# Performance work log

Measured on AMD Instinct MI355X. Metric: run time of the kernel, lower is better.

The kernel has to match this reference:

```python
import jax, jax.numpy as jnp
import numpy as np
import math

B, D_MODEL, EMB, ORDER, SEQ = 4, 64, 33, 64, 256
TARGET, FAST_PCT, SLOW_PCT = 0.01, 0.3, 1.5


def _pos_emb(L, emb_dim):
    # PositionalEmbedding: t in [0,1], complex exponential bands
    t = jnp.linspace(0.0, 1.0, L)[None, :, None]                     # [1,L,1]
    bands = (emb_dim - 1) // 2
    t_r = jnp.linspace(0.0, L - 1.0, L)[None, :, None]
    w = 2.0 * math.pi * t_r / L
    f = jnp.linspace(1e-4, bands - 1.0, bands)[None, None]
    zc = jnp.exp(-1j * f * w)
    z = jnp.concatenate([t, zc.real, zc.imag], axis=-1)              # [1,L,emb_dim]
    return z.astype(jnp.float32), t.astype(jnp.float32)


def setup_inputs() -> dict:
    key = jax.random.key(0)
    ks = jax.random.split(key, 24)
    z, _ = _pos_emb(SEQ, EMB)

    def lin(k, fan_in, fan_out):
        return jax.random.normal(k, (fan_in, fan_out), jnp.float32) / np.sqrt(fan_in)

    inp = {
        'x': jax.random.normal(ks[0], (B, D_MODEL, SEQ, SEQ), jnp.float32),
        'z': z,
        'Xw1': lin(ks[1], EMB, ORDER), 'Xb1': jax.random.normal(ks[2], (ORDER,), jnp.float32) * 0.02,
        'Xw2': lin(ks[3], ORDER, ORDER), 'Xb2': jax.random.normal(ks[4], (ORDER,), jnp.float32) * 0.02,
        'Xw3': lin(ks[5], ORDER, ORDER), 'Xb3': jax.random.normal(ks[6], (ORDER,), jnp.float32) * 0.02,
        'Xwo': lin(ks[7], ORDER, D_MODEL),
        'Xfreq': jnp.ones((1, ORDER), jnp.float32),  # Sin freq, w=1, shared across layers
        'Yw1': lin(ks[8], EMB, ORDER), 'Yb1': jax.random.normal(ks[9], (ORDER,), jnp.float32) * 0.02,
        'Yw2': lin(ks[10], ORDER, ORDER), 'Yb2': jax.random.normal(ks[11], (ORDER,), jnp.float32) * 0.02,
        'Yw3': lin(ks[12], ORDER, ORDER), 'Yb3': jax.random.normal(ks[13], (ORDER,), jnp.float32) * 0.02,
        'Ywo': lin(ks[14], ORDER, D_MODEL),
        'Yfreq': jnp.ones((1, ORDER), jnp.float32),
        'bias': jax.random.normal(ks[15], (D_MODEL,), jnp.float32),
        'L': SEQ,
    }
    return inp


def _implicit_filter(z, w1, b1, w2, b2, w3, b3, wo, freq, t, deltas):
    # MLP with shared Sin activation, then exponential modulation (shift=0)
    h = jnp.sin(freq * (z @ w1 + b1))
    h = jnp.sin(freq * (h @ w2 + b2))
    h = jnp.sin(freq * (h @ w3 + b3))
    h = h @ wo                                   # [1,L,d_model]
    decay = jnp.exp(-t * jnp.abs(deltas))        # [1,L,d_model]
    return h * decay


def reference(x, z, Xw1, Xb1, Xw2, Xb2, Xw3, Xb3, Xwo, Xfreq,
              Yw1, Yb1, Yw2, Yb2, Yw3, Yb3, Ywo, Yfreq, bias, L):
    d_model = x.shape[1]
    t = jnp.linspace(0.0, 1.0, L)[None, :, None].astype(jnp.float32)
    max_dec = math.log(TARGET) / FAST_PCT
    min_dec = math.log(TARGET) / SLOW_PCT
    deltas = jnp.linspace(min_dec, max_dec, d_model)[None, None].astype(jnp.float32)

    hx = _implicit_filter(z, Xw1, Xb1, Xw2, Xb2, Xw3, Xb3, Xwo, Xfreq, t, deltas)
    hy = _implicit_filter(z, Yw1, Yb1, Yw2, Yb2, Yw3, Yb3, Ywo, Yfreq, t, deltas)
    # separable outer-product 2D kernel: [1,L,L,d_model] -> [d_model,L,L]
    k = jnp.einsum('ijk,imk->ijmk', hx, hy)[0]
    k = jnp.transpose(k, (2, 0, 1))

    fft_size = 2 * L
    k_f = jnp.fft.rfft2(k, s=(fft_size, fft_size)) / fft_size       # [D, 2L, L+1]
    u_f = jnp.fft.rfft2(x.astype(jnp.float32), s=(fft_size, fft_size))  # [B, D, 2L, L+1]
    y = jnp.fft.irfft2(u_f * k_f, s=(fft_size, fft_size))[..., :L, :L]
    out = y + x * bias[:, None, None]
    return out.astype(x.dtype)
```

## Files before the change

kernel.cpp:

```cpp
#include <hip/hip_runtime.h>

#define SL 256

typedef _Float16 f16;
typedef _Float16 f16x8 __attribute__((ext_vector_type(8)));
typedef _Float16 f16x4 __attribute__((ext_vector_type(4)));
typedef float f32x4 __attribute__((ext_vector_type(4)));

__global__ __launch_bounds__(64) void k_filters(
    const float* __restrict__ z,
    const float* __restrict__ Xw1, const float* __restrict__ Xb1,
    const float* __restrict__ Xw2, const float* __restrict__ Xb2,
    const float* __restrict__ Xw3, const float* __restrict__ Xb3,
    const float* __restrict__ Xwo, const float* __restrict__ Xfreq,
    const float* __restrict__ Yw1, const float* __restrict__ Yb1,
    const float* __restrict__ Yw2, const float* __restrict__ Yb2,
    const float* __restrict__ Yw3, const float* __restrict__ Yb3,
    const float* __restrict__ Ywo, const float* __restrict__ Yfreq,
    float* __restrict__ hx, float* __restrict__ hy)
{
    const int l = blockIdx.x;
    const int sel = blockIdx.y;
    const int t = threadIdx.x;
    const float* w1 = sel ? Yw1 : Xw1;  const float* b1 = sel ? Yb1 : Xb1;
    const float* w2 = sel ? Yw2 : Xw2;  const float* b2 = sel ? Yb2 : Xb2;
    const float* w3 = sel ? Yw3 : Xw3;  const float* b3 = sel ? Yb3 : Xb3;
    const float* wo = sel ? Ywo : Xwo;  const float* freq = sel ? Yfreq : Xfreq;
    float* hout = sel ? hy : hx;

    __shared__ float zb[33];
    __shared__ float ha[64];
    __shared__ float hb[64];

    if (t < 33) zb[t] = z[l * 33 + t];
    __syncthreads();

    const float fr = freq[t];
    float s = b1[t];
    for (int k = 0; k < 33; ++k) s += zb[k] * w1[k * 64 + t];
    ha[t] = sinf(fr * s);
    __syncthreads();

    s = b2[t];
    for (int k = 0; k < 64; ++k) s += ha[k] * w2[k * 64 + t];
    hb[t] = sinf(fr * s);
    __syncthreads();

    s = b3[t];
    for (int k = 0; k < 64; ++k) s += hb[k] * w3[k * 64 + t];
    ha[t] = sinf(fr * s);
    __syncthreads();

    s = 0.f;
    for (int k = 0; k < 64; ++k) s += ha[k] * wo[k * 64 + t];

    const float MIN_DEC = -3.0701134573253937f;
    const float MAX_DEC = -15.350567286626968f;
    float ad = fabsf(MIN_DEC + (MAX_DEC - MIN_DEC) * ((float)t / 63.0f));
    float tl = (float)l / 255.0f;
    hout[l * 64 + t] = s * expf(-tl * ad);
}

__device__ __forceinline__ void build_R(f16* R, const float* __restrict__ hcol,
                                        int d, int tid)
{
    for (int idx = tid; idx < 8 * 520; idx += 1024) {
        int c = idx / 520;
        int k = idx - c * 520;
        int u = k + c;
        float v = (u <= 255) ? hcol[(255 - u) * 64 + d] : 0.f;
        R[idx] = (f16)v;
    }
}

__global__ __launch_bounds__(1024, 4) void k_fused(
    const float* __restrict__ x, const float* __restrict__ hx,
    const float* __restrict__ hy, const float* __restrict__ bias,
    float* __restrict__ out)
{
    const int bd = blockIdx.x;
    const int d  = bd & 63;
    const int tid  = threadIdx.x;
    const int lane = tid & 63;
    const int wave = tid >> 6;
    const int ln   = lane & 15;
    const int quad = lane >> 4;

    __shared__ __align__(16) f16 tmp[256 * 256];
    __shared__ __align__(16) f16 R[8 * 520];

    const float* xbd = x + (size_t)bd * (SL * SL);

    build_R(R, hy, d, tid);

    f32x4 acc[16];
#pragma unroll
    for (int a = 0; a < 16; ++a) acc[a] = (f32x4){0.f, 0.f, 0.f, 0.f};

    __syncthreads();

    {
        const int wp = wave & 3;
        const int wj = wave >> 2;

        float4 pv0[4], pv1[4];
#pragma unroll
        for (int rt = 0; rt < 4; ++rt) {
            const float* src = xbd + (wp * 64 + rt * 16 + ln) * SL + quad * 8;
            pv0[rt] = *(const float4*)src;
            pv1[rt] = *(const float4*)(src + 4);
        }

        for (int q0 = 0; q0 < 256; q0 += 32) {
            f16x8 af[4], bf[4];
#pragma unroll
            for (int rt = 0; rt < 4; ++rt) {
                f16x8 h;
                h[0] = (f16)pv0[rt].x; h[1] = (f16)pv0[rt].y;
                h[2] = (f16)pv0[rt].z; h[3] = (f16)pv0[rt].w;
                h[4] = (f16)pv1[rt].x; h[5] = (f16)pv1[rt].y;
                h[6] = (f16)pv1[rt].z; h[7] = (f16)pv1[rt].w;
                af[rt] = h;
            }
            if (q0 < 224) {
#pragma unroll
                for (int rt = 0; rt < 4; ++rt) {
                    const float* src = xbd + (wp * 64 + rt * 16 + ln) * SL
                                     + q0 + 32 + quad * 8;
                    pv0[rt] = *(const float4*)src;
                    pv1[rt] = *(const float4*)(src + 4);
                }
            }
#pragma unroll
            for (int ct = 0; ct < 4; ++ct) {
                int j = wj * 64 + ct * 16 + ln;
                int s0 = 255 - j + q0 + quad * 8;
                int c = s0 & 7;
                bf[ct] = *(const f16x8*)&R[c * 520 + (s0 - c)];
            }
#pragma unroll
            for (int rt = 0; rt < 4; ++rt)
#pragma unroll
                for (int ct = 0; ct < 4; ++ct)
                    acc[rt * 4 + ct] = __builtin_amdgcn_mfma_f32_16x16x32_f16(
                        af[rt], bf[ct], acc[rt * 4 + ct], 0, 0, 0);
        }

#pragma unroll
        for (int rt = 0; rt < 4; ++rt)
#pragma unroll
            for (int ct = 0; ct < 4; ++ct) {
                int j = wj * 64 + ct * 16 + ln;
                int pb = wp * 64 + rt * 16 + quad * 4;
                f32x4 a = acc[rt * 4 + ct];
                f16x4 v;
                v[0] = (f16)a[0]; v[1] = (f16)a[1];
                v[2] = (f16)a[2]; v[3] = (f16)a[3];
                *(f16x4*)&tmp[j * 256 + (pb ^ ((j & 7) << 3))] = v;
            }
    }

    __syncthreads();
    build_R(R, hx, d, tid);
#pragma unroll
    for (int a = 0; a < 16; ++a) acc[a] = (f32x4){0.f, 0.f, 0.f, 0.f};
    __syncthreads();

    const int wii = wave & 3;
    const int wjj = wave >> 2;
    for (int p0 = 0; p0 < 256; p0 += 32) {
        f16x8 af[4], bf[4];
#pragma unroll
        for (int rt = 0; rt < 4; ++rt) {
            int j = wjj * 64 + rt * 16 + ln;
            int off = (p0 + quad * 8) ^ ((j & 7) << 3);
            af[rt] = *(const f16x8*)&tmp[j * 256 + off];
        }
#pragma unroll
        for (int ct = 0; ct < 4; ++ct) {
            int i = wii * 64 + ct * 16 + ln;
            int s0 = 255 - i + p0 + quad * 8;
            int c = s0 & 7;
            bf[ct] = *(const f16x8*)&R[c * 520 + (s0 - c)];
        }
#pragma unroll
        for (int rt = 0; rt < 4; ++rt)
#pragma unroll
            for (int ct = 0; ct < 4; ++ct)
                acc[rt * 4 + ct] = __builtin_amdgcn_mfma_f32_16x16x32_f16(
                    af[rt], bf[ct], acc[rt * 4 + ct], 0, 0, 0);
    }

    const float bv = bias[d];
    const float sc = 1.0f / 512.0f;
    float* obd = out + (size_t)bd * (SL * SL);
#pragma unroll
    for (int rt = 0; rt < 4; ++rt)
#pragma unroll
        for (int ct = 0; ct < 4; ++ct) {
            int i  = wii * 64 + ct * 16 + ln;
            int jb = wjj * 64 + rt * 16 + quad * 4;
            f32x4 a = acc[rt * 4 + ct];
            float4 xv = *(const float4*)(xbd + i * SL + jb);
            float4 o;
            o.x = a[0] * sc + xv.x * bv;
            o.y = a[1] * sc + xv.y * bv;
            o.z = a[2] * sc + xv.z * bv;
            o.w = a[3] * sc + xv.w * bv;
            *(float4*)(obd + i * SL + jb) = o;
        }
}

extern "C" void kernel_launch(void* const* d_in, const int* in_sizes, int n_in,
                              void* d_out, int out_size, void* d_ws, size_t ws_size,
                              hipStream_t stream)
{
    (void)in_sizes; (void)n_in; (void)out_size; (void)ws_size;
    const float* x     = (const float*)d_in[0];
    const float* z     = (const float*)d_in[1];
    const float* Xw1   = (const float*)d_in[2];
    const float* Xb1   = (const float*)d_in[3];
    const float* Xw2   = (const float*)d_in[4];
    const float* Xb2   = (const float*)d_in[5];
    const float* Xw3   = (const float*)d_in[6];
    const float* Xb3   = (const float*)d_in[7];
    const float* Xwo   = (const float*)d_in[8];
    const float* Xfreq = (const float*)d_in[9];
    const float* Yw1   = (const float*)d_in[10];
    const float* Yb1   = (const float*)d_in[11];
    const float* Yw2   = (const float*)d_in[12];
    const float* Yb2   = (const float*)d_in[13];
    const float* Yw3   = (const float*)d_in[14];
    const float* Yb3   = (const float*)d_in[15];
    const float* Ywo   = (const float*)d_in[16];
    const float* Yfreq = (const float*)d_in[17];
    const float* bias  = (const float*)d_in[18];

    float* hx = (float*)d_ws;
    float* hy = hx + 256 * 64;

    k_filters<<<dim3(256, 2), 64, 0, stream>>>(
        z, Xw1, Xb1, Xw2, Xb2, Xw3, Xb3, Xwo, Xfreq,
        Yw1, Yb1, Yw2, Yb2, Yw3, Yb3, Ywo, Yfreq, hx, hy);
    k_fused<<<256, 1024, 0, stream>>>(x, hx, hy, bias, (float*)d_out);
}
```

Measured before the change: 192.4 us.

## Retile first Toeplitz GEMM per wave, store filters transposed fp16, prefetch x

The filter kernel now writes hx/hy transposed in fp16, so both Toeplitz staging buffers (Rx, Ry) are built in one pass with contiguous loads and one fewer barrier. In the first GEMM each wave now owns a 16-row strip across all 256 columns, with a 3-deep register prefetch of x, instead of a 64x64 tile. The second GEMM interleaves B-fragment loads with MFMAs, and the x values for the bias epilogue are prefetched before and during the MMA loop. This trades more LDS B-fragment reads in stage one and extra LDS for Rx, which may affect occupancy, for less global latency and simpler setup.

```diff
diff --git a/kernel.cpp b/kernel.cpp
--- a/kernel.cpp
+++ b/kernel.cpp
@@ -17,7 +17,7 @@
     const float* __restrict__ Yw2, const float* __restrict__ Yb2,
     const float* __restrict__ Yw3, const float* __restrict__ Yb3,
     const float* __restrict__ Ywo, const float* __restrict__ Yfreq,
-    float* __restrict__ hx, float* __restrict__ hy)
+    f16* __restrict__ hxT, f16* __restrict__ hyT)
 {
     const int l = blockIdx.x;
     const int sel = blockIdx.y;
@@ -26,7 +26,7 @@
     const float* w2 = sel ? Yw2 : Xw2;  const float* b2 = sel ? Yb2 : Xb2;
     const float* w3 = sel ? Yw3 : Xw3;  const float* b3 = sel ? Yb3 : Xb3;
     const float* wo = sel ? Ywo : Xwo;  const float* freq = sel ? Yfreq : Xfreq;
-    float* hout = sel ? hy : hx;
+    f16* hT = sel ? hyT : hxT;
 
     __shared__ float zb[33];
     __shared__ float ha[64];
@@ -58,24 +58,20 @@
     const float MAX_DEC = -15.350567286626968f;
     float ad = fabsf(MIN_DEC + (MAX_DEC - MIN_DEC) * ((float)t / 63.0f));
     float tl = (float)l / 255.0f;
-    hout[l * 64 + t] = s * expf(-tl * ad);
-}
-
-__device__ __forceinline__ void build_R(f16* R, const float* __restrict__ hcol,
-                                        int d, int tid)
-{
-    for (int idx = tid; idx < 8 * 520; idx += 1024) {
-        int c = idx / 520;
-        int k = idx - c * 520;
-        int u = k + c;
-        float v = (u <= 255) ? hcol[(255 - u) * 64 + d] : 0.f;
-        R[idx] = (f16)v;
-    }
+    hT[t * 256 + l] = (f16)(s * expf(-tl * ad));
+}
+
+__device__ __forceinline__ f16x8 cvt8(float4 a, float4 b)
+{
+    f16x8 h;
+    h[0] = (f16)a.x; h[1] = (f16)a.y; h[2] = (f16)a.z; h[3] = (f16)a.w;
+    h[4] = (f16)b.x; h[5] = (f16)b.y; h[6] = (f16)b.z; h[7] = (f16)b.w;
+    return h;
 }
 
 __global__ __launch_bounds__(1024, 4) void k_fused(
-    const float* __restrict__ x, const float* __restrict__ hx,
-    const float* __restrict__ hy, const float* __restrict__ bias,
+    const float* __restrict__ x, const f16* __restrict__ hxT,
+    const f16* __restrict__ hyT, const float* __restrict__ bias,
     float* __restrict__ out)
 {
     const int bd = blockIdx.x;
@@ -87,11 +83,30 @@
     const int quad = lane >> 4;
 
     __shared__ __align__(16) f16 tmp[256 * 256];
-    __shared__ __align__(16) f16 R[8 * 520];
+    __shared__ __align__(16) f16 Ry[8 * 520];
+    __shared__ __align__(16) f16 Rx[8 * 520];
 
     const float* xbd = x + (size_t)bd * (SL * SL);
-
-    build_R(R, hy, d, tid);
+    const float* xrow = xbd + (wave * 16 + ln) * SL + quad * 8;
+
+    float4 pfa[8], pfb[8];
+#pragma unroll
+    for (int s = 0; s < 3; ++s) {
+        pfa[s] = *(const float4*)(xrow + s * 32);
+        pfb[s] = *(const float4*)(xrow + s * 32 + 4);
+    }
+
+    const f16* hyc = hyT + d * 256;
+    const f16* hxc = hxT + d * 256;
+    for (int idx = tid; idx < 8 * 520; idx += 1024) {
+        int c = idx / 520;
+        int k = idx - c * 520;
+        int u = k + c;
+        f16 vy = (f16)0.f, vx = (f16)0.f;
+        if (u <= 255) { vy = hyc[255 - u]; vx = hxc[255 - u]; }
+        Ry[idx] = vy;
+        Rx[idx] = vx;
+    }
 
     f32x4 acc[16];
 #pragma unroll
@@ -99,77 +114,62 @@
 
     __syncthreads();
 
-    {
-        const int wp = wave & 3;
-        const int wj = wave >> 2;
-
-        float4 pv0[4], pv1[4];
-#pragma unroll
-        for (int rt = 0; rt < 4; ++rt) {
-            const float* src = xbd + (wp * 64 + rt * 16 + ln) * SL + quad * 8;
-            pv0[rt] = *(const float4*)src;
-            pv1[rt] = *(const float4*)(src + 4);
-        }
-
-        for (int q0 = 0; q0 < 256; q0 += 32) {
-            f16x8 af[4], bf[4];
-#pragma unroll
-            for (int rt = 0; rt < 4; ++rt) {
-                f16x8 h;
-                h[0] = (f16)pv0[rt].x; h[1] = (f16)pv0[rt].y;
-                h[2] = (f16)pv0[rt].z; h[3] = (f16)pv0[rt].w;
-                h[4] = (f16)pv1[rt].x; h[5] = (f16)pv1[rt].y;
-                h[6] = (f16)pv1[rt].z; h[7] = (f16)pv1[rt].w;
-                af[rt] = h;
-            }
-            if (q0 < 224) {
-#pragma unroll
-                for (int rt = 0; rt < 4; ++rt) {
-                    const float* src = xbd + (wp * 64 + rt * 16 + ln) * SL
-                                     + q0 + 32 + quad * 8;
-                    pv0[rt] = *(const float4*)src;
-                    pv1[rt] = *(const float4*)(src + 4);
-                }
-            }
-#pragma unroll
-            for (int ct = 0; ct < 4; ++ct) {
-                int j = wj * 64 + ct * 16 + ln;
+#pragma unroll
+    for (int s = 0; s < 8; ++s) {
+        const int q0 = s * 32;
+        if (s + 3 < 8) {
+            pfa[s + 3] = *(const float4*)(xrow + (s + 3) * 32);
+            pfb[s + 3] = *(const float4*)(xrow + (s + 3) * 32 + 4);
+        }
+        f16x8 af = cvt8(pfa[s], pfb[s]);
+#pragma unroll
+        for (int h = 0; h < 2; ++h) {
+            f16x8 bf[8];
+#pragma unroll
+            for (int c8 = 0; c8 < 8; ++c8) {
+                int j = (h * 8 + c8) * 16 + ln;
                 int s0 = 255 - j + q0 + quad * 8;
                 int c = s0 & 7;
-                bf[ct] = *(const f16x8*)&R[c * 520 + (s0 - c)];
+                bf[c8] = *(const f16x8*)&Ry[c * 520 + (s0 - c)];
             }
 #pragma unroll
-            for (int rt = 0; rt < 4; ++rt)
-#pragma unroll
-                for (int ct = 0; ct < 4; ++ct)
-                    acc[rt * 4 + ct] = __builtin_amdgcn_mfma_f32_16x16x32_f16(
-                        af[rt], bf[ct], acc[rt * 4 + ct], 0, 0, 0);
-        }
-
-#pragma unroll
-        for (int rt = 0; rt < 4; ++rt)
-#pragma unroll
-            for (int ct = 0; ct < 4; ++ct) {
-                int j = wj * 64 + ct * 16 + ln;
-                int pb = wp * 64 + rt * 16 + quad * 4;
-                f32x4 a = acc[rt * 4 + ct];
-                f16x4 v;
-                v[0] = (f16)a[0]; v[1] = (f16)a[1];
-                v[2] = (f16)a[2]; v[3] = (f16)a[3];
-                *(f16x4*)&tmp[j * 256 + (pb ^ ((j & 7) << 3))] = v;
-            }
-    }
-
-    __syncthreads();
-    build_R(R, hx, d, tid);
+            for (int c8 = 0; c8 < 8; ++c8)
+                acc[h * 8 + c8] = __builtin_amdgcn_mfma_f32_16x16x32_f16(
+                    af, bf[c8], acc[h * 8 + c8], 0, 0, 0);
+        }
+    }
+
+    {
+        const int pb = wave * 16 + quad * 4;
+#pragma unroll
+        for (int ct = 0; ct < 16; ++ct) {
+            int j = ct * 16 + ln;
+            f32x4 a = acc[ct];
+            f16x4 v;
+            v[0] = (f16)a[0]; v[1] = (f16)a[1];
+            v[2] = (f16)a[2]; v[3] = (f16)a[3];
+            *(f16x4*)&tmp[j * 256 + (pb ^ ((j & 7) << 3))] = v;
+        }
+    }
+
+    __syncthreads();
+
 #pragma unroll
     for (int a = 0; a < 16; ++a) acc[a] = (f32x4){0.f, 0.f, 0.f, 0.f};
-    __syncthreads();
 
     const int wii = wave & 3;
     const int wjj = wave >> 2;
+
+    float4 xpf[8];
+#pragma unroll
+    for (int g = 0; g < 2; ++g)
+#pragma unroll
+        for (int rt = 0; rt < 4; ++rt)
+            xpf[g * 4 + rt] = *(const float4*)(xbd
+                + (wii * 64 + g * 16 + ln) * SL + wjj * 64 + rt * 16 + quad * 4);
+
     for (int p0 = 0; p0 < 256; p0 += 32) {
-        f16x8 af[4], bf[4];
+        f16x8 af[4];
 #pragma unroll
         for (int rt = 0; rt < 4; ++rt) {
             int j = wjj * 64 + rt * 16 + ln;
@@ -181,27 +181,48 @@
             int i = wii * 64 + ct * 16 + ln;
             int s0 = 255 - i + p0 + quad * 8;
             int c = s0 & 7;
-            bf[ct] = *(const f16x8*)&R[c * 520 + (s0 - c)];
-        }
+            f16x8 bf = *(const f16x8*)&Rx[c * 520 + (s0 - c)];
+#pragma unroll
+            for (int rt = 0; rt < 4; ++rt)
+                acc[rt * 4 + ct] = __builtin_amdgcn_mfma_f32_16x16x32_f16(
+                    af[rt], bf, acc[rt * 4 + ct], 0, 0, 0);
+        }
+    }
+
+    float4 xp2[8];
+#pragma unroll
+    for (int g = 0; g < 2; ++g)
 #pragma unroll
         for (int rt = 0; rt < 4; ++rt)
-#pragma unroll
-            for (int ct = 0; ct < 4; ++ct)
-                acc[rt * 4 + ct] = __builtin_amdgcn_mfma_f32_16x16x32_f16(
-                    af[rt], bf[ct], acc[rt * 4 + ct], 0, 0, 0);
-    }
+            xp2[g * 4 + rt] = *(const float4*)(xbd
+                + (wii * 64 + (g + 2) * 16 + ln) * SL + wjj * 64 + rt * 16 + quad * 4);
 
     const float bv = bias[d];
     const float sc = 1.0f / 512.0f;
     float* obd = out + (size_t)bd * (SL * SL);
 #pragma unroll
-    for (int rt = 0; rt < 4; ++rt)
-#pragma unroll
-        for (int ct = 0; ct < 4; ++ct) {
-            int i  = wii * 64 + ct * 16 + ln;
+    for (int g = 0; g < 2; ++g)
+#pragma unroll
+        for (int rt = 0; rt < 4; ++rt) {
+            int i  = wii * 64 + g * 16 + ln;
             int jb = wjj * 64 + rt * 16 + quad * 4;
-            f32x4 a = acc[rt * 4 + ct];
-            float4 xv = *(const float4*)(xbd + i * SL + jb);
+            f32x4 a = acc[rt * 4 + g];
+            float4 xv = xpf[g * 4 + rt];
+            float4 o;
+            o.x = a[0] * sc + xv.x * bv;
+            o.y = a[1] * sc + xv.y * bv;
+            o.z = a[2] * sc + xv.z * bv;
+            o.w = a[3] * sc + xv.w * bv;
+            *(float4*)(obd + i * SL + jb) = o;
+        }
+#pragma unroll
+    for (int g = 0; g < 2; ++g)
+#pragma unroll
+        for (int rt = 0; rt < 4; ++rt) {
+            int i  = wii * 64 + (g + 2) * 16 + ln;
+            int jb = wjj * 64 + rt * 16 + quad * 4;
+            f32x4 a = acc[rt * 4 + (g + 2)];
+            float4 xv = xp2[g * 4 + rt];
             float4 o;
             o.x = a[0] * sc + xv.x * bv;
             o.y = a[1] * sc + xv.y * bv;
@@ -236,11 +257,11 @@
     const float* Yfreq = (const float*)d_in[17];
     const float* bias  = (const float*)d_in[18];
 
-    float* hx = (float*)d_ws;
-    float* hy = hx + 256 * 64;
+    f16* hxT = (f16*)d_ws;
+    f16* hyT = hxT + 64 * 256;
 
     k_filters<<<dim3(256, 2), 64, 0, stream>>>(
         z, Xw1, Xb1, Xw2, Xb2, Xw3, Xb3, Xwo, Xfreq,
-        Yw1, Yb1, Yw2, Yb2, Yw3, Yb3, Ywo, Yfreq, hx, hy);
-    k_fused<<<256, 1024, 0, stream>>>(x, hx, hy, bias, (float*)d_out);
-}
+        Yw1, Yb1, Yw2, Yb2, Yw3, Yb3, Ywo, Yfreq, hxT, hyT);
+    k_fused<<<256, 1024, 0, stream>>>(x, hxT, hyT, bias, (float*)d_out);
+}
```

After: 256.5 us. +33.3%, slower.
